# Optimization experiments

Hardware: AMD Instinct MI355X
Metric: run time of the kernel (lower is better)

The kernel has to match this reference:

```python
import jax, jax.numpy as jnp
import numpy as np

DEGREE = 3        # self.degree = 3 in MGNN
K = 3             # Chebyshev/polynomial order of the GCN
BANDWIDTH = 512.0 # Gaussian kernel bandwidth (~2*d so adj spans (0,1])
B, N, D_IN = 2, 4096, 256
D_OUT = 64        # 2*D_OUT == 128 == linear output dim


def _bspline(t, degree):
    """Cox-de Boor recursive B-spline basis N_{0,degree}(t), elementwise,
    uniform knots on [0,1]. t: [B,N,N] adjacency values."""
    knots = np.linspace(0.0, 1.0, degree + 2)  # static python floats
    basis = [jnp.where((t >= knots[i]) & (t < knots[i + 1]), 1.0, 0.0).astype(t.dtype)
             for i in range(degree + 1)]
    for k in range(1, degree + 1):
        basis = [
            (t - knots[i]) / (knots[i + k] - knots[i]) * basis[i]
            + (knots[i + k + 1] - t) / (knots[i + k + 1] - knots[i + 1]) * basis[i + 1]
            for i in range(degree + 1 - k)
        ]
    return basis[0]


def _wavelet(t, degree):
    # spline wavelet: difference of dilated/shifted B-splines
    return _bspline(2.0 * t, degree) - _bspline(2.0 * t - 1.0, degree)


def _graph_construction(x, bandwidth):
    # Gaussian-kernel dense adjacency per batch element: [B,N,N], values in (0,1]
    sq = jnp.sum(x * x, axis=-1)                                   # [B,N]
    d2 = sq[:, :, None] + sq[:, None, :] - 2.0 * jnp.einsum('bnd,bmd->bnm', x, x)
    d2 = jnp.maximum(d2, 0.0)
    return jnp.exp(-d2 / bandwidth)


def _gcn(x, kernel, Wk):
    # out = sum_k (kernel^k x) W_k ; Wk: [K, D_IN, D_OUT]
    h = x
    out = jnp.einsum('bnd,do->bno', h, Wk[0])
    for k in range(1, Wk.shape[0]):
        h = jnp.einsum('bnm,bmd->bnd', kernel, h)
        out = out + jnp.einsum('bnd,do->bno', h, Wk[k])
    return out


def setup_inputs() -> dict:
    key = jax.random.key(0)
    k0, k1, k2, k3 = jax.random.split(key, 4)
    x = jax.random.normal(k0, (B, N, D_IN), dtype=jnp.float32)
    Wk = jax.random.normal(k1, (K, D_IN, D_OUT), dtype=jnp.float32) * 0.05
    W_lin = jax.random.normal(k2, (D_IN, 2 * D_OUT), dtype=jnp.float32) * 0.05
    b_lin = jnp.zeros((2 * D_OUT,), dtype=jnp.float32)
    return {"x": x, "Wk": Wk, "W_lin": W_lin, "b_lin": b_lin}


def reference(x, Wk, W_lin, b_lin):
    adj = _graph_construction(x, BANDWIDTH)       # [B,N,N]
    b_kernel = _bspline(adj, DEGREE)              # [B,N,N]
    w_kernel = _wavelet(adj, DEGREE)              # [B,N,N]
    gcn1 = _gcn(x, b_kernel, Wk)                  # [B,N,D_OUT]
    gcn2 = _gcn(x, w_kernel, Wk)                  # [B,N,D_OUT]
    akgcn = jnp.concatenate([gcn1, gcn2], axis=-1)        # [B,N,2*D_OUT]
    akgcn = jax.nn.relu(akgcn + x @ W_lin + b_lin)        # residual + relu
    return akgcn.reshape(akgcn.shape[0], -1)              # flatten last two dims
```

## Files before the change

kernel.cpp:

```cpp
#include <hip/hip_runtime.h>
#include <hip/hip_bf16.h>

typedef __hip_bfloat16 bf16;
typedef float v4f __attribute__((ext_vector_type(4)));
typedef short v8s __attribute__((ext_vector_type(8)));
typedef unsigned u32;

typedef const __attribute__((address_space(1))) void gvoid;
typedef __attribute__((address_space(3))) void lvoid;

__device__ __forceinline__ void async16(const void* g, void* l) {
  __builtin_amdgcn_global_load_lds((gvoid*)g, (lvoid*)l, 16, 0, 0);
}

__device__ __forceinline__ unsigned short f2bf(float v) {
  __hip_bfloat16 h = __float2bfloat16(v);
  return *(unsigned short*)&h;
}
__device__ __forceinline__ float bflo(u32 dw) {
  u32 u = dw << 16;
  return *(float*)&u;
}
__device__ __forceinline__ float bfhi(u32 dw) {
  u32 u = dw & 0xffff0000u;
  return *(float*)&u;
}

__device__ __forceinline__ float b3(float u) {
  u = fminf(fmaxf(u, 0.f), 4.f);
  float t1 = fmaxf(u - 1.f, 0.f);
  float t2 = fmaxf(u - 2.f, 0.f);
  float t3 = fmaxf(u - 3.f, 0.f);
  float c0 = u * u * u;
  float c1 = t1 * t1 * t1;
  float c2 = t2 * t2 * t2;
  float c3 = t3 * t3 * t3;
  return (c0 - 4.f * c1 + 6.f * c2 - 4.f * c3) * (1.f / 6.f);
}

template <int NI, int BK>
__device__ __forceinline__ void mfma_loop(const bf16* __restrict__ A,
                                          const bf16* __restrict__ B, int lda,
                                          int ldb, int kLen, bf16* As, bf16* Bs,
                                          v4f acc[4][NI]) {
  const int tid = threadIdx.x;
  const int wave = tid >> 6;
  const int lane = tid & 63;
  const int quad = lane >> 4;
  const int r16 = lane & 15;
  const int wm = (wave >> 1) * 64;
  const int wn = (wave & 1) * (NI * 16);
  constexpr int CPR = BK / 8;
  constexpr int AQ = 128 * CPR / 256;
  constexpr int BQ = NI * 32 * CPR / 256;
  char* AsC = (char*)As;
  char* BsC = (char*)Bs;
  for (int kk = 0; kk < kLen; kk += BK) {
#pragma unroll
    for (int q = 0; q < AQ; ++q) {
      const int ch = tid + 256 * q;
      const int r = ch / CPR, c = (ch % CPR) * 8;
      async16(A + (size_t)r * lda + kk + c, AsC + q * 4096 + wave * 1024);
    }
#pragma unroll
    for (int q = 0; q < BQ; ++q) {
      const int ch = tid + 256 * q;
      const int r = ch / CPR, c = (ch % CPR) * 8;
      async16(B + (size_t)r * ldb + kk + c, BsC + q * 4096 + wave * 1024);
    }
    __syncthreads();
#pragma unroll
    for (int ks = 0; ks < BK / 32; ++ks) {
      v8s af[4], bfr[NI];
#pragma unroll
      for (int mi = 0; mi < 4; ++mi)
        af[mi] =
            *(const v8s*)(As + (wm + mi * 16 + r16) * BK + ks * 32 + quad * 8);
#pragma unroll
      for (int ni = 0; ni < NI; ++ni)
        bfr[ni] =
            *(const v8s*)(Bs + (wn + ni * 16 + r16) * BK + ks * 32 + quad * 8);
#pragma unroll
      for (int mi = 0; mi < 4; ++mi)
#pragma unroll
        for (int ni = 0; ni < NI; ++ni)
          acc[mi][ni] = __builtin_amdgcn_mfma_f32_16x16x32_bf16(
              af[mi], bfr[ni], acc[mi][ni], 0, 0, 0);
    }
    __syncthreads();
  }
}

__global__ void prep(const float* __restrict__ x, bf16* __restrict__ U,
                     float* __restrict__ sq) {
  const int n = blockIdx.x, b = blockIdx.y, t = threadIdx.x;
  const size_t row = (size_t)b * 4096 + n;
  float v = x[row * 256 + t];
  U[row * 1280 + t] = __float2bfloat16(v);
  float s = v * v;
#pragma unroll
  for (int o = 32; o > 0; o >>= 1) s += __shfl_down(s, o, 64);
  __shared__ float ls[4];
  if ((t & 63) == 0) ls[t >> 6] = s;
  __syncthreads();
  if (t == 0) sq[row] = ls[0] + ls[1] + ls[2] + ls[3];
}

__global__ void transk(const float* __restrict__ src, bf16* __restrict__ dst) {
  __shared__ float tile[64][65];
  const int z = blockIdx.z;
  const float* s = src + (size_t)z * 4096 * 256;
  bf16* d = dst + (size_t)z * 256 * 4096;
  const int n0 = blockIdx.x * 64, d0 = blockIdx.y * 64;
  const int tx = threadIdx.x & 31, ty = threadIdx.x >> 5;
#pragma unroll
  for (int i = 0; i < 8; ++i) {
    const int r = ty + i * 8;
    const float2 v = *(const float2*)(s + (size_t)(n0 + r) * 256 + d0 + tx * 2);
    tile[r][tx * 2] = v.x;
    tile[r][tx * 2 + 1] = v.y;
  }
  __syncthreads();
#pragma unroll
  for (int i = 0; i < 8; ++i) {
    const int c = ty + i * 8;
    __hip_bfloat162 p;
    p.x = __float2bfloat16(tile[tx * 2][c]);
    p.y = __float2bfloat16(tile[tx * 2 + 1][c]);
    *(__hip_bfloat162*)(d + (size_t)(d0 + c) * 4096 + n0 + tx * 2) = p;
  }
}

__global__ void wbig(const float* __restrict__ Wk, const float* __restrict__ Wl,
                     bf16* __restrict__ WbT) {
  int idx = blockIdx.x * 256 + threadIdx.x;
  if (idx >= 128 * 1280) return;
  int j = idx / 1280, k = idx % 1280;
  int o = j & 63;
  float v = 0.f;
  if (k < 256)
    v = Wk[k * 64 + o] + Wl[k * 128 + j];
  else if (k < 512)
    v = (j < 64) ? Wk[16384 + (k - 256) * 64 + o] : 0.f;
  else if (k < 768)
    v = (j < 64) ? Wk[32768 + (k - 512) * 64 + o] : 0.f;
  else if (k < 1024)
    v = (j >= 64) ? Wk[16384 + (k - 768) * 64 + o] : 0.f;
  else
    v = (j >= 64) ? Wk[32768 + (k - 1024) * 64 + o] : 0.f;
  WbT[idx] = __float2bfloat16(v);
}

__global__ __launch_bounds__(256, 2) void gemm_s(const bf16* __restrict__ U,
                                                 const float* __restrict__ sq,
                                                 unsigned short* __restrict__ kbw) {
  __shared__ __align__(16) bf16 As[128 * 64];
  __shared__ __align__(16) bf16 Bs[128 * 64];
  __shared__ u32 lut[2048];
  const int tid = threadIdx.x;
  for (int i = tid; i < 2048; i += 256) {
    float t = (i + 0.5f) * (1.f / 2048.f);
    float bv = b3(4.f * t);
    float wv = b3(8.f * t) - b3(8.f * t - 4.f);
    u32 bq = (u32)fminf(bv * 382.5f + 0.5f, 255.f);
    u32 wq = (u32)fminf((wv + 2.f / 3.f) * 191.25f + 0.5f, 255.f);
    lut[i] = bq | (wq << 8);
  }
  const int z = blockIdx.z;
  const bf16* A = U + (size_t)z * 4096 * 1280 + (size_t)blockIdx.x * 128 * 1280;
  const bf16* B = U + (size_t)z * 4096 * 1280 + (size_t)blockIdx.y * 128 * 1280;
  v4f acc[4][4];
#pragma unroll
  for (int a = 0; a < 4; ++a)
#pragma unroll
    for (int b2 = 0; b2 < 4; ++b2) acc[a][b2] = (v4f){0.f, 0.f, 0.f, 0.f};
  mfma_loop<4, 64>(A, B, 1280, 1280, 256, As, Bs, acc);
  const int wave = tid >> 6, lane = tid & 63;
  const int quad = lane >> 4, r16 = lane & 15;
  const int wm = (wave >> 1) * 64, wn = (wave & 1) * 64;
  const float* sqr = sq + (size_t)z * 4096;
  unsigned short* ks = kbw + (size_t)z * 4096 * 4096;
  const int i0 = blockIdx.x * 128 + wm + quad * 4;
  const int j0 = blockIdx.y * 128 + wn + r16;
  const int par = lane & 1;
  const int jc = j0 - par;
  float sqj[4];
#pragma unroll
  for (int ni = 0; ni < 4; ++ni) sqj[ni] = sqr[j0 + ni * 16];
  const float c = -1.4426950408889634f / 512.f;
#pragma unroll
  for (int mi = 0; mi < 4; ++mi) {
#pragma unroll
    for (int ni = 0; ni < 4; ++ni) {
      u32 pv[4];
#pragma unroll
      for (int r = 0; r < 4; ++r) {
        float s = acc[mi][ni][r];
        float d2 = fmaxf(sqr[i0 + mi * 16 + r] + sqj[ni] - 2.f * s, 0.f);
        float t = __builtin_amdgcn_exp2f(d2 * c);
        int idx = (int)fminf(t * 2048.f, 2047.f);
        pv[r] = lut[idx];
      }
      u32 ov[4];
#pragma unroll
      for (int r = 0; r < 4; ++r) ov[r] = __shfl_xor((int)pv[r], 1, 64);
#pragma unroll
      for (int rr = 0; rr < 2; ++rr) {
        const int r = par * 2 + rr;
        const u32 a = pv[r], b2 = ov[r];
        const u32 lo = par ? b2 : a;
        const u32 hi = par ? a : b2;
        const int i = i0 + mi * 16 + r;
        const size_t off = (size_t)i * 4096 + jc + ni * 16;
        *(u32*)(ks + off) = (lo & 0xffffu) | (hi << 16);
      }
    }
  }
}

template <int KERN>
__device__ __forceinline__ void hloop(const unsigned short* __restrict__ A,
                                      const bf16* __restrict__ B,
                                      unsigned short* Ar, bf16* Bs,
                                      v4f acc[4][4]) {
  constexpr float KSC = KERN ? (4.f / 3.f / 255.f) : (2.f / 3.f / 255.f);
  constexpr float KOF = KERN ? (-2.f / 3.f) : 0.f;
  const int tid = threadIdx.x;
  const int wave = tid >> 6, lane = tid & 63;
  const int quad = lane >> 4, r16 = lane & 15;
  const int wm = (wave >> 1) * 64, wn = (wave & 1) * 64;
  char* ArC = (char*)Ar;
  char* BsC = (char*)Bs;
  for (int kk = 0; kk < 1024; kk += 64) {
#pragma unroll
    for (int q = 0; q < 4; ++q) {
      const int ch = tid + 256 * q;
      const int r = ch >> 3, c8 = (ch & 7) * 8;
      async16(A + (size_t)r * 4096 + kk + c8, ArC + q * 4096 + wave * 1024);
    }
#pragma unroll
    for (int q = 0; q < 4; ++q) {
      const int ch = tid + 256 * q;
      const int r = ch >> 3, c8 = (ch & 7) * 8;
      async16(B + (size_t)r * 4096 + kk + c8, BsC + q * 4096 + wave * 1024);
    }
    __syncthreads();
#pragma unroll
    for (int ks = 0; ks < 2; ++ks) {
      v8s af[4], bfr[4];
#pragma unroll
      for (int mi = 0; mi < 4; ++mi) {
        const uint4 raw = *(const uint4*)(Ar + (wm + mi * 16 + r16) * 64 +
                                          ks * 32 + quad * 8);
        const u32 din[4] = {raw.x, raw.y, raw.z, raw.w};
        union {
          u32 d[4];
          v8s s;
        } cv;
#pragma unroll
        for (int d = 0; d < 4; ++d) {
          const u32 dw = din[d];
          float f0, f1;
          if (KERN == 0) {
            f0 = (float)(dw & 0xffu) * KSC;
            f1 = (float)((dw >> 16) & 0xffu) * KSC;
          } else {
            f0 = (float)((dw >> 8) & 0xffu) * KSC + KOF;
            f1 = (float)(dw >> 24) * KSC + KOF;
          }
          cv.d[d] = __builtin_amdgcn_perm(__float_as_uint(f1),
                                          __float_as_uint(f0), 0x07060302u);
        }
        af[mi] = cv.s;
      }
#pragma unroll
      for (int ni = 0; ni < 4; ++ni)
        bfr[ni] =
            *(const v8s*)(Bs + (wn + ni * 16 + r16) * 64 + ks * 32 + quad * 8);
#pragma unroll
      for (int mi = 0; mi < 4; ++mi)
#pragma unroll
        for (int ni = 0; ni < 4; ++ni)
          acc[mi][ni] = __builtin_amdgcn_mfma_f32_16x16x32_bf16(
              af[mi], bfr[ni], acc[mi][ni], 0, 0, 0);
    }
    __syncthreads();
  }
}

__global__ __launch_bounds__(256, 4) void gemm_h(
    const unsigned short* __restrict__ kbw, const bf16* __restrict__ BtBase,
    bf16* __restrict__ hpart, int btShift) {
  __shared__ __align__(16) unsigned short Ar[128 * 64];
  __shared__ __align__(16) bf16 Bs[128 * 64];
  const int bz = blockIdx.z;
  const int z = bz >> 2, split = bz & 3;
  const int batch = z >> 1, kern = z & 1;
  const int kk0 = split * 1024;
  const unsigned short* A = kbw + (size_t)batch * 4096 * 4096 +
                            (size_t)blockIdx.x * 128 * 4096 + kk0;
  const bf16* B = BtBase + (size_t)(z >> btShift) * 256 * 4096 +
                  (size_t)blockIdx.y * 128 * 4096 + kk0;
  v4f acc[4][4];
#pragma unroll
  for (int a = 0; a < 4; ++a)
#pragma unroll
    for (int b2 = 0; b2 < 4; ++b2) acc[a][b2] = (v4f){0.f, 0.f, 0.f, 0.f};
  if (kern == 0)
    hloop<0>(A, B, Ar, Bs, acc);
  else
    hloop<1>(A, B, Ar, Bs, acc);
  const int tid = threadIdx.x, wave = tid >> 6, lane = tid & 63;
  const int quad = lane >> 4, r16 = lane & 15;
  const int wm = (wave >> 1) * 64, wn = (wave & 1) * 64;
  bf16* H = hpart + ((size_t)split * 4 + z) * 4096 * 256;
  const int i0 = blockIdx.x * 128 + wm + quad * 4;
  const int j0 = blockIdx.y * 128 + wn + r16;
  const int par = lane & 1;
  const int jc = j0 - par;
#pragma unroll
  for (int mi = 0; mi < 4; ++mi) {
#pragma unroll
    for (int ni = 0; ni < 4; ++ni) {
      u32 pv[4];
#pragma unroll
      for (int r = 0; r < 4; ++r) pv[r] = (u32)f2bf(acc[mi][ni][r]);
      u32 ov[4];
#pragma unroll
      for (int r = 0; r < 4; ++r) ov[r] = __shfl_xor((int)pv[r], 1, 64);
#pragma unroll
      for (int rr = 0; rr < 2; ++rr) {
        const int r = par * 2 + rr;
        const u32 a = pv[r], b2 = ov[r];
        const u32 lo = par ? b2 : a;
        const u32 hi = par ? a : b2;
        const int i = i0 + mi * 16 + r;
        *(u32*)(H + (size_t)i * 256 + jc + ni * 16) = lo | (hi << 16);
      }
    }
  }
}

__global__ void reduceT(const bf16* __restrict__ hpart, bf16* __restrict__ U,
                        bf16* __restrict__ hT, int uoffBase) {
  __shared__ float tile[64][65];
  const int z = blockIdx.z;
  const int b = z >> 1, kern = z & 1;
  const int uoff = uoffBase + kern * 512;
  const int n0 = blockIdx.x * 64, d0 = blockIdx.y * 64;
  const int tx = threadIdx.x & 31, ty = threadIdx.x >> 5;
  const size_t sstride = (size_t)4 * 4096 * 256;
  const bf16* s0 = hpart + (size_t)z * 4096 * 256;
#pragma unroll
  for (int i = 0; i < 8; ++i) {
    const int r = ty + i * 8;
    const size_t off = (size_t)(n0 + r) * 256 + d0 + tx * 2;
    float vx = 0.f, vy = 0.f;
#pragma unroll
    for (int k = 0; k < 4; ++k) {
      const u32 dw = *(const u32*)(s0 + k * sstride + off);
      vx += bflo(dw);
      vy += bfhi(dw);
    }
    tile[r][tx * 2] = vx;
    tile[r][tx * 2 + 1] = vy;
    __hip_bfloat162 p;
    p.x = __float2bfloat16(vx);
    p.y = __float2bfloat16(vy);
    *(__hip_bfloat162*)(U + (size_t)(b * 4096 + n0 + r) * 1280 + uoff + d0 +
                        tx * 2) = p;
  }
  if (hT) {
    __syncthreads();
#pragma unroll
    for (int i = 0; i < 8; ++i) {
      const int c = ty + i * 8;
      __hip_bfloat162 p;
      p.x = __float2bfloat16(tile[tx * 2][c]);
      p.y = __float2bfloat16(tile[tx * 2 + 1][c]);
      *(__hip_bfloat162*)(hT + (size_t)z * 256 * 4096 + (size_t)(d0 + c) * 4096 +
                          n0 + tx * 2) = p;
    }
  }
}

__global__ __launch_bounds__(256, 4) void gemm_proj(
    const bf16* __restrict__ U, const bf16* __restrict__ WbT,
    const float* __restrict__ blin, float* __restrict__ out) {
  __shared__ __align__(16) bf16 As[128 * 64];
  __shared__ __align__(16) bf16 Bs[64 * 64];
  const bf16* A = U + (size_t)blockIdx.x * 128 * 1280;
  const bf16* B = WbT + (size_t)blockIdx.y * 64 * 1280;
  v4f acc[4][2];
#pragma unroll
  for (int a = 0; a < 4; ++a)
#pragma unroll
    for (int b2 = 0; b2 < 2; ++b2) acc[a][b2] = (v4f){0.f, 0.f, 0.f, 0.f};
  mfma_loop<2, 64>(A, B, 1280, 1280, 1280, As, Bs, acc);
  const int tid = threadIdx.x, wave = tid >> 6, lane = tid & 63;
  const int quad = lane >> 4, r16 = lane & 15;
  const int wm = (wave >> 1) * 64, wn = (wave & 1) * 32;
  const int i0 = blockIdx.x * 128 + wm + quad * 4;
  const int j0 = blockIdx.y * 64 + wn + r16;
#pragma unroll
  for (int mi = 0; mi < 4; ++mi)
#pragma unroll
    for (int r = 0; r < 4; ++r) {
      const int i = i0 + mi * 16 + r;
#pragma unroll
      for (int ni = 0; ni < 2; ++ni) {
        const int j = j0 + ni * 16;
        out[(size_t)i * 128 + j] = fmaxf(acc[mi][ni][r] + blin[j], 0.f);
      }
    }
}

extern "C" void kernel_launch(void* const* d_in, const int* in_sizes, int n_in,
                              void* d_out, int out_size, void* d_ws,
                              size_t ws_size, hipStream_t stream) {
  const float* x = (const float*)d_in[0];
  const float* Wk = (const float*)d_in[1];
  const float* Wlin = (const float*)d_in[2];
  const float* blin = (const float*)d_in[3];
  float* out = (float*)d_out;
  char* w = (char*)d_ws;
  unsigned short* kbw = (unsigned short*)(w);
  bf16* hpart = (bf16*)(w + 67108864);
  bf16* h1T = (bf16*)(w + 100663296);
  bf16* xhT = (bf16*)(w + 109051904);
  bf16* U = (bf16*)(w + 113246208);
  bf16* WbT = (bf16*)(w + 134217728);
  float* sqv = (float*)(w + 134545408);

  prep<<<dim3(4096, 2), 256, 0, stream>>>(x, U, sqv);
  transk<<<dim3(64, 4, 2), 256, 0, stream>>>(x, xhT);
  wbig<<<dim3(640), 256, 0, stream>>>(Wk, Wlin, WbT);
  gemm_s<<<dim3(32, 32, 2), 256, 0, stream>>>(U, sqv, kbw);
  gemm_h<<<dim3(32, 2, 16), 256, 0, stream>>>(kbw, xhT, hpart, 1);
  reduceT<<<dim3(64, 4, 4), 256, 0, stream>>>(hpart, U, h1T, 256);
  gemm_h<<<dim3(32, 2, 16), 256, 0, stream>>>(kbw, h1T, hpart, 0);
  reduceT<<<dim3(64, 4, 4), 256, 0, stream>>>(hpart, U, nullptr, 512);
  gemm_proj<<<dim3(64, 2), 256, 0, stream>>>(U, WbT, blin, out);
}
```

Measured before the change: 244.9 us.

## Fuse both kernels in first hop GEMM and XOR-swizzle LDS tiles

Adds gemm_h2, which handles the first propagation hop for both the B-spline and wavelet kernels in one block. It loads each packed adjacency tile and each x tile once and feeds two accumulator sets, halving A/B global traffic and launch count for that hop. Separately, all LDS tile loads and reads now use an XOR swizzle of the 16-byte chunk index by row, to avoid LDS bank conflicts on the fragment reads. The cost is double the accumulator registers (launch bounds lowered to 2 blocks per CU), so occupancy drops.

```diff
diff --git a/kernel.cpp b/kernel.cpp
--- a/kernel.cpp
+++ b/kernel.cpp
@@ -24,6 +24,10 @@
 __device__ __forceinline__ float bfhi(u32 dw) {
   u32 u = dw & 0xffff0000u;
   return *(float*)&u;
+}
+__device__ __forceinline__ u32 packbf(float f0, float f1) {
+  return __builtin_amdgcn_perm(__float_as_uint(f1), __float_as_uint(f0),
+                               0x07060302u);
 }
 
 __device__ __forceinline__ float b3(float u) {
@@ -53,19 +57,22 @@
   constexpr int CPR = BK / 8;
   constexpr int AQ = 128 * CPR / 256;
   constexpr int BQ = NI * 32 * CPR / 256;
+  constexpr int MSK = CPR - 1;
   char* AsC = (char*)As;
   char* BsC = (char*)Bs;
   for (int kk = 0; kk < kLen; kk += BK) {
 #pragma unroll
     for (int q = 0; q < AQ; ++q) {
       const int ch = tid + 256 * q;
-      const int r = ch / CPR, c = (ch % CPR) * 8;
+      const int r = ch / CPR;
+      const int c = ((ch & MSK) ^ (r & MSK)) * 8;
       async16(A + (size_t)r * lda + kk + c, AsC + q * 4096 + wave * 1024);
     }
 #pragma unroll
     for (int q = 0; q < BQ; ++q) {
       const int ch = tid + 256 * q;
-      const int r = ch / CPR, c = (ch % CPR) * 8;
+      const int r = ch / CPR;
+      const int c = ((ch & MSK) ^ (r & MSK)) * 8;
       async16(B + (size_t)r * ldb + kk + c, BsC + q * 4096 + wave * 1024);
     }
     __syncthreads();
@@ -73,13 +80,17 @@
     for (int ks = 0; ks < BK / 32; ++ks) {
       v8s af[4], bfr[NI];
 #pragma unroll
-      for (int mi = 0; mi < 4; ++mi)
-        af[mi] =
-            *(const v8s*)(As + (wm + mi * 16 + r16) * BK + ks * 32 + quad * 8);
-#pragma unroll
-      for (int ni = 0; ni < NI; ++ni)
-        bfr[ni] =
-            *(const v8s*)(Bs + (wn + ni * 16 + r16) * BK + ks * 32 + quad * 8);
+      for (int mi = 0; mi < 4; ++mi) {
+        const int row = wm + mi * 16 + r16;
+        const int cc = ((ks * 4 + quad) ^ (row & MSK)) * 8;
+        af[mi] = *(const v8s*)(As + row * BK + cc);
+      }
+#pragma unroll
+      for (int ni = 0; ni < NI; ++ni) {
+        const int row = wn + ni * 16 + r16;
+        const int cc = ((ks * 4 + quad) ^ (row & MSK)) * 8;
+        bfr[ni] = *(const v8s*)(Bs + row * BK + cc);
+      }
 #pragma unroll
       for (int mi = 0; mi < 4; ++mi)
 #pragma unroll
@@ -218,6 +229,129 @@
   }
 }
 
+__device__ __forceinline__ void store_partial(const v4f acc[4][4],
+                                              bf16* __restrict__ H, int i0,
+                                              int jc, int par) {
+#pragma unroll
+  for (int mi = 0; mi < 4; ++mi) {
+#pragma unroll
+    for (int ni = 0; ni < 4; ++ni) {
+      u32 pv[4];
+#pragma unroll
+      for (int r = 0; r < 4; ++r) pv[r] = (u32)f2bf(acc[mi][ni][r]);
+      u32 ov[4];
+#pragma unroll
+      for (int r = 0; r < 4; ++r) ov[r] = __shfl_xor((int)pv[r], 1, 64);
+#pragma unroll
+      for (int rr = 0; rr < 2; ++rr) {
+        const int r = par * 2 + rr;
+        const u32 a = pv[r], b2 = ov[r];
+        const u32 lo = par ? b2 : a;
+        const u32 hi = par ? a : b2;
+        const int i = i0 + mi * 16 + r;
+        *(u32*)(H + (size_t)i * 256 + jc + ni * 16) = lo | (hi << 16);
+      }
+    }
+  }
+}
+
+__global__ __launch_bounds__(256, 2) void gemm_h2(
+    const unsigned short* __restrict__ kbw, const bf16* __restrict__ xhT,
+    bf16* __restrict__ hpart) {
+  __shared__ __align__(16) unsigned short Ar[128 * 64];
+  __shared__ __align__(16) bf16 Bs[128 * 64];
+  const int batch = blockIdx.z >> 2, split = blockIdx.z & 3;
+  const int kk0 = split * 1024;
+  const unsigned short* A = kbw + (size_t)batch * 4096 * 4096 +
+                            (size_t)blockIdx.x * 128 * 4096 + kk0;
+  const bf16* B = xhT + (size_t)batch * 256 * 4096 +
+                  (size_t)blockIdx.y * 128 * 4096 + kk0;
+  constexpr float S0 = 2.f / 3.f / 255.f;
+  constexpr float S1 = 4.f / 3.f / 255.f;
+  constexpr float O1 = -2.f / 3.f;
+  const int tid = threadIdx.x;
+  const int wave = tid >> 6, lane = tid & 63;
+  const int quad = lane >> 4, r16 = lane & 15;
+  const int wm = (wave >> 1) * 64, wn = (wave & 1) * 64;
+  char* ArC = (char*)Ar;
+  char* BsC = (char*)Bs;
+  v4f acc0[4][4], acc1[4][4];
+#pragma unroll
+  for (int a = 0; a < 4; ++a)
+#pragma unroll
+    for (int b2 = 0; b2 < 4; ++b2) {
+      acc0[a][b2] = (v4f){0.f, 0.f, 0.f, 0.f};
+      acc1[a][b2] = (v4f){0.f, 0.f, 0.f, 0.f};
+    }
+  for (int kk = 0; kk < 1024; kk += 64) {
+#pragma unroll
+    for (int q = 0; q < 4; ++q) {
+      const int ch = tid + 256 * q;
+      const int r = ch >> 3;
+      const int c8 = (((ch & 7) ^ (r & 7))) * 8;
+      async16(A + (size_t)r * 4096 + kk + c8, ArC + q * 4096 + wave * 1024);
+    }
+#pragma unroll
+    for (int q = 0; q < 4; ++q) {
+      const int ch = tid + 256 * q;
+      const int r = ch >> 3;
+      const int c8 = (((ch & 7) ^ (r & 7))) * 8;
+      async16(B + (size_t)r * 4096 + kk + c8, BsC + q * 4096 + wave * 1024);
+    }
+    __syncthreads();
+#pragma unroll
+    for (int ks = 0; ks < 2; ++ks) {
+      v8s bfr[4];
+#pragma unroll
+      for (int ni = 0; ni < 4; ++ni) {
+        const int row = wn + ni * 16 + r16;
+        const int cc = ((ks * 4 + quad) ^ (row & 7)) * 8;
+        bfr[ni] = *(const v8s*)(Bs + row * 64 + cc);
+      }
+#pragma unroll
+      for (int mi = 0; mi < 4; ++mi) {
+        const int row = wm + mi * 16 + r16;
+        const int cc = ((ks * 4 + quad) ^ (row & 7)) * 8;
+        const uint4 raw = *(const uint4*)(Ar + row * 64 + cc);
+        const u32 din[4] = {raw.x, raw.y, raw.z, raw.w};
+        union {
+          u32 d[4];
+          v8s s;
+        } cv;
+#pragma unroll
+        for (int d = 0; d < 4; ++d) {
+          const u32 dw = din[d];
+          cv.d[d] = packbf((float)(dw & 0xffu) * S0,
+                           (float)((dw >> 16) & 0xffu) * S0);
+        }
+#pragma unroll
+        for (int ni = 0; ni < 4; ++ni)
+          acc0[mi][ni] = __builtin_amdgcn_mfma_f32_16x16x32_bf16(
+              cv.s, bfr[ni], acc0[mi][ni], 0, 0, 0);
+#pragma unroll
+        for (int d = 0; d < 4; ++d) {
+          const u32 dw = din[d];
+          cv.d[d] = packbf((float)((dw >> 8) & 0xffu) * S1 + O1,
+                           (float)(dw >> 24) * S1 + O1);
+        }
+#pragma unroll
+        for (int ni = 0; ni < 4; ++ni)
+          acc1[mi][ni] = __builtin_amdgcn_mfma_f32_16x16x32_bf16(
+              cv.s, bfr[ni], acc1[mi][ni], 0, 0, 0);
+      }
+    }
+    __syncthreads();
+  }
+  const int i0 = blockIdx.x * 128 + wm + quad * 4;
+  const int j0 = blockIdx.y * 128 + wn + r16;
+  const int par = lane & 1;
+  const int jc = j0 - par;
+  bf16* H0 = hpart + ((size_t)split * 4 + batch * 2 + 0) * 4096 * 256;
+  bf16* H1 = hpart + ((size_t)split * 4 + batch * 2 + 1) * 4096 * 256;
+  store_partial(acc0, H0, i0, jc, par);
+  store_partial(acc1, H1, i0, jc, par);
+}
+
 template <int KERN>
 __device__ __forceinline__ void hloop(const unsigned short* __restrict__ A,
                                       const bf16* __restrict__ B,
@@ -235,13 +369,15 @@
 #pragma unroll
     for (int q = 0; q < 4; ++q) {
       const int ch = tid + 256 * q;
-      const int r = ch >> 3, c8 = (ch & 7) * 8;
+      const int r = ch >> 3;
+      const int c8 = (((ch & 7) ^ (r & 7))) * 8;
       async16(A + (size_t)r * 4096 + kk + c8, ArC + q * 4096 + wave * 1024);
     }
 #pragma unroll
     for (int q = 0; q < 4; ++q) {
       const int ch = tid + 256 * q;
-      const int r = ch >> 3, c8 = (ch & 7) * 8;
+      const int r = ch >> 3;
+      const int c8 = (((ch & 7) ^ (r & 7))) * 8;
       async16(B + (size_t)r * 4096 + kk + c8, BsC + q * 4096 + wave * 1024);
     }
     __syncthreads();
@@ -250,8 +386,9 @@
       v8s af[4], bfr[4];
 #pragma unroll
       for (int mi = 0; mi < 4; ++mi) {
-        const uint4 raw = *(const uint4*)(Ar + (wm + mi * 16 + r16) * 64 +
-                                          ks * 32 + quad * 8);
+        const int row = wm + mi * 16 + r16;
+        const int cc = ((ks * 4 + quad) ^ (row & 7)) * 8;
+        const uint4 raw = *(const uint4*)(Ar + row * 64 + cc);
         const u32 din[4] = {raw.x, raw.y, raw.z, raw.w};
         union {
           u32 d[4];
@@ -268,15 +405,16 @@
             f0 = (float)((dw >> 8) & 0xffu) * KSC + KOF;
             f1 = (float)(dw >> 24) * KSC + KOF;
           }
-          cv.d[d] = __builtin_amdgcn_perm(__float_as_uint(f1),
-                                          __float_as_uint(f0), 0x07060302u);
+          cv.d[d] = packbf(f0, f1);
         }
         af[mi] = cv.s;
       }
 #pragma unroll
-      for (int ni = 0; ni < 4; ++ni)
-        bfr[ni] =
-            *(const v8s*)(Bs + (wn + ni * 16 + r16) * 64 + ks * 32 + quad * 8);
+      for (int ni = 0; ni < 4; ++ni) {
+        const int row = wn + ni * 16 + r16;
+        const int cc = ((ks * 4 + quad) ^ (row & 7)) * 8;
+        bfr[ni] = *(const v8s*)(Bs + row * 64 + cc);
+      }
 #pragma unroll
       for (int mi = 0; mi < 4; ++mi)
 #pragma unroll
@@ -290,7 +428,7 @@
 
 __global__ __launch_bounds__(256, 4) void gemm_h(
     const unsigned short* __restrict__ kbw, const bf16* __restrict__ BtBase,
-    bf16* __restrict__ hpart, int btShift) {
+    bf16* __restrict__ hpart) {
   __shared__ __align__(16) unsigned short Ar[128 * 64];
   __shared__ __align__(16) bf16 Bs[128 * 64];
   const int bz = blockIdx.z;
@@ -299,8 +437,8 @@
   const int kk0 = split * 1024;
   const unsigned short* A = kbw + (size_t)batch * 4096 * 4096 +
                             (size_t)blockIdx.x * 128 * 4096 + kk0;
-  const bf16* B = BtBase + (size_t)(z >> btShift) * 256 * 4096 +
-                  (size_t)blockIdx.y * 128 * 4096 + kk0;
+  const bf16* B =
+      BtBase + (size_t)z * 256 * 4096 + (size_t)blockIdx.y * 128 * 4096 + kk0;
   v4f acc[4][4];
 #pragma unroll
   for (int a = 0; a < 4; ++a)
@@ -318,27 +456,7 @@
   const int j0 = blockIdx.y * 128 + wn + r16;
   const int par = lane & 1;
   const int jc = j0 - par;
-#pragma unroll
-  for (int mi = 0; mi < 4; ++mi) {
-#pragma unroll
-    for (int ni = 0; ni < 4; ++ni) {
-      u32 pv[4];
-#pragma unroll
-      for (int r = 0; r < 4; ++r) pv[r] = (u32)f2bf(acc[mi][ni][r]);
-      u32 ov[4];
-#pragma unroll
-      for (int r = 0; r < 4; ++r) ov[r] = __shfl_xor((int)pv[r], 1, 64);
-#pragma unroll
-      for (int rr = 0; rr < 2; ++rr) {
-        const int r = par * 2 + rr;
-        const u32 a = pv[r], b2 = ov[r];
-        const u32 lo = par ? b2 : a;
-        const u32 hi = par ? a : b2;
-        const int i = i0 + mi * 16 + r;
-        *(u32*)(H + (size_t)i * 256 + jc + ni * 16) = lo | (hi << 16);
-      }
-    }
-  }
+  store_partial(acc, H, i0, jc, par);
 }
 
 __global__ void reduceT(const bf16* __restrict__ hpart, bf16* __restrict__ U,
@@ -436,9 +554,9 @@
   transk<<<dim3(64, 4, 2), 256, 0, stream>>>(x, xhT);
   wbig<<<dim3(640), 256, 0, stream>>>(Wk, Wlin, WbT);
   gemm_s<<<dim3(32, 32, 2), 256, 0, stream>>>(U, sqv, kbw);
-  gemm_h<<<dim3(32, 2, 16), 256, 0, stream>>>(kbw, xhT, hpart, 1);
+  gemm_h2<<<dim3(32, 2, 8), 256, 0, stream>>>(kbw, xhT, hpart);
   reduceT<<<dim3(64, 4, 4), 256, 0, stream>>>(hpart, U, h1T, 256);
-  gemm_h<<<dim3(32, 2, 16), 256, 0, stream>>>(kbw, h1T, hpart, 0);
+  gemm_h<<<dim3(32, 2, 16), 256, 0, stream>>>(kbw, h1T, hpart);
   reduceT<<<dim3(64, 4, 4), 256, 0, stream>>>(hpart, U, nullptr, 512);
   gemm_proj<<<dim3(64, 2), 256, 0, stream>>>(U, WbT, blin, out);
 }
```

After: 257.8 us. +5.3%, slower.
